# Kernel optimization log

Hardware: AMD Instinct MI355X
Metric: run time of the kernel (lower is better)

The kernel has to match this reference:

```python
import jax, jax.numpy as jnp
import numpy as np

N_NODES = 50000
N_EDGES = 800000
D_NODE = 64
D_ATTR = 16
D_T = 16
D_OUT = 128


def setup_inputs() -> dict:
    key = jax.random.key(0)
    ks = jax.random.split(key, 8)
    x = jax.random.normal(ks[0], (N_NODES, D_NODE), dtype=jnp.float32)
    edge_index = jax.random.randint(ks[1], (2, N_EDGES), 0, N_NODES, dtype=jnp.int64)
    edge_attr = jax.random.normal(ks[2], (N_EDGES, D_ATTR), dtype=jnp.float32)
    edge_t = jax.random.normal(ks[3], (N_EDGES, D_T), dtype=jnp.float32)
    d_msg = D_NODE + D_ATTR + D_T  # 96, = in_channels[0]
    Wm = jax.random.normal(ks[4], (d_msg, D_OUT), dtype=jnp.float32) / np.sqrt(d_msg)
    bm = jnp.zeros((D_OUT,), dtype=jnp.float32)
    Wr = jax.random.normal(ks[5], (D_NODE, D_OUT), dtype=jnp.float32) / np.sqrt(D_NODE)
    br = jnp.zeros((D_OUT,), dtype=jnp.float32)
    return {"x": x, "edge_index": edge_index, "edge_attr": edge_attr,
            "edge_t": edge_t, "Wm": Wm, "bm": bm, "Wr": Wr, "br": br}


def reference(x, edge_index, edge_attr, edge_t, Wm, bm, Wr, br):
    row, col = edge_index[0], edge_index[1]
    # gather source node feats and concat edge features -> [E, 96]
    msg = jnp.concatenate([x[col], edge_attr, edge_t], axis=1)
    # scatter-sum messages to destination nodes -> [N, 96]
    agg = jax.ops.segment_sum(msg, row, num_segments=x.shape[0])
    x_j = agg @ Wm + bm          # lin_m
    x_i = x @ Wr + br            # lin_r
    out = 0.5 * x_j + x_i        # normalize=False path
    return out
```

## Files before the change

### kernel.cpp

```cpp
#include <hip/hip_runtime.h>
#include <hip/hip_bf16.h>

#define NN 50000
#define NE 800000
#define D_NODE 64
#define D_MSG 96
#define D_K 160
#define AS 192
#define D_OUT 128
#define KP 168

#define SCAN_BLOCKS 49
#define XCAST_BLOCKS 3125
#define BT_BLOCKS 80

typedef __attribute__((ext_vector_type(8))) short bf16x8;
typedef __attribute__((ext_vector_type(4))) float f32x4;

#define CNT_OFF  0
#define DONE_OFF 200000
#define OFF_OFF  200064
#define CUR_OFF  400064
#define PERM_OFF 600064
#define A_OFF    7000064
#define BSUM_OFF (A_OFF + 128)

__device__ __forceinline__ unsigned short f2bf(float f) {
    __hip_bfloat16 h = __float2bfloat16(f);
    union { __hip_bfloat16 h; unsigned short u; } c; c.h = h;
    return c.u;
}
__device__ __forceinline__ float bf2f(unsigned int u) {
    union { unsigned int i; float f; } c; c.i = u << 16; return c.f;
}

__global__ __launch_bounds__(256) void prep_kernel(
    const float* __restrict__ x, unsigned short* __restrict__ A,
    const int* __restrict__ row, int* __restrict__ cnt)
{
    const int b = blockIdx.x;
    if (b < XCAST_BLOCKS) {
        int i = b * 256 + threadIdx.x;
        int node = i >> 4, c4 = i & 15;
        float4 v = *(const float4*)(x + (size_t)node * D_NODE + c4 * 4);
        uint2 pk;
        pk.x = (unsigned)f2bf(v.x) | ((unsigned)f2bf(v.y) << 16);
        pk.y = (unsigned)f2bf(v.z) | ((unsigned)f2bf(v.w) << 16);
        *(uint2*)(A + (size_t)node * AS + c4 * 4) = pk;
    } else {
        int e = (b - XCAST_BLOCKS) * 256 + threadIdx.x;
        if (e < NE) atomicAdd(&cnt[row[e]], 1);
    }
}

__global__ __launch_bounds__(256) void scan_kernel(
    const int* __restrict__ cnt, int* __restrict__ bsum,
    int* __restrict__ off, int* __restrict__ cur, int* __restrict__ done)
{
    const int t = threadIdx.x, b = blockIdx.x;
    const int idx4 = b * 256 + t;
    const bool valid = (idx4 < NN / 4);

    __shared__ int wsumA[4];
    int4 c = make_int4(0, 0, 0, 0);
    if (valid) c = ((const int4*)cnt)[idx4];
    int s = c.x + c.y + c.z + c.w;
    {
        int r = s;
        for (int d = 32; d > 0; d >>= 1) r += __shfl_down(r, d);
        if ((t & 63) == 0) wsumA[t >> 6] = r;
    }
    __syncthreads();
    if (t == 0) {
        bsum[b] = wsumA[0] + wsumA[1] + wsumA[2] + wsumA[3];
        __threadfence();
        atomicAdd(done, 1);
        while (__hip_atomic_load(done, __ATOMIC_ACQUIRE,
                                 __HIP_MEMORY_SCOPE_AGENT) < SCAN_BLOCKS)
            __builtin_amdgcn_s_sleep(1);
    }
    __syncthreads();

    __shared__ int s_boff;
    __shared__ int wsumC[4];
    if (t < 64) {
        int v = (t < SCAN_BLOCKS) ? bsum[t] : 0;
        int orig = v;
        for (int d = 1; d < 64; d <<= 1) {
            int u = __shfl_up(v, d);
            if (t >= d) v += u;
        }
        int excl = v - orig;
        int want = __shfl(excl, b);
        if (t == 0) s_boff = want;
    }

    const int lane = t & 63, w = t >> 6;
    int v = s;
    for (int d = 1; d < 64; d <<= 1) {
        int u = __shfl_up(v, d);
        if (lane >= d) v += u;
    }
    if (lane == 63) wsumC[w] = v;
    __syncthreads();
    int woff = 0;
    for (int i = 0; i < 4; ++i) if (i < w) woff += wsumC[i];

    if (valid) {
        int excl = (v - s) + woff + s_boff;
        int4 o;
        o.x = excl;
        o.y = o.x + c.x;
        o.z = o.y + c.y;
        o.w = o.z + c.z;
        ((int4*)off)[idx4] = o;
        ((int4*)cur)[idx4] = o;
    }
}

__global__ __launch_bounds__(256) void bucket_kernel(
    const int* __restrict__ row, const int* __restrict__ col,
    int* __restrict__ cur, int2* __restrict__ perm)
{
    int e = blockIdx.x * blockDim.x + threadIdx.x;
    if (e >= NE) return;
    int pos = atomicAdd(&cur[row[e]], 1);
    perm[pos] = make_int2(e, col[e]);
}

__global__ __launch_bounds__(256) void gather_kernel(
    const float* __restrict__ ea,
    const float* __restrict__ et,
    const int*  __restrict__ off,
    const int*  __restrict__ cnt,
    const int2* __restrict__ perm,
    unsigned short* __restrict__ A,
    const float* __restrict__ Wm,
    const float* __restrict__ Wr,
    unsigned short* __restrict__ Bt)
{
    const int grp = blockIdx.x;
    if (grp >= NN / 4) {
        int idx = (grp - NN / 4) * 256 + threadIdx.x;
        int n = idx & 127, k = idx >> 7;
        float v = (k < D_NODE) ? Wr[k * D_OUT + n] : Wm[(k - D_NODE) * D_OUT + n];
        Bt[n * KP + k] = f2bf(v);
        return;
    }

    const int node = grp * 4 + (threadIdx.x >> 6);
    const int lane = threadIdx.x & 63;

    const int beg = off[node];
    const int end = beg + cnt[node];

    const int half = lane >> 5;
    const int hl   = lane & 31;
    const float* ebase = ((lane >> 4) & 1) ? et : ea;
    const int ecol = lane & 15;

    float accx0 = 0.f, accx1 = 0.f, acce = 0.f;
    float accx0b = 0.f, accx1b = 0.f, acceb = 0.f;

#define EDGE_PAIR(q, ax0, ax1, ae)                                          \
    {                                                                       \
        int cc = half ? (q).w : (q).y;                                      \
        int ee = half ? (q).z : (q).x;                                      \
        unsigned xv = *(const unsigned*)(A + (size_t)cc * AS + hl * 2);     \
        float ev = ebase[(size_t)ee * 16 + ecol];                           \
        ax0 += bf2f(xv & 0xffffu);                                          \
        ax1 += bf2f(xv >> 16);                                              \
        ae  += ev;                                                          \
    }

    int j = beg;
    if ((j & 1) && j < end) {
        int2 p = perm[j];
        if (half == 0) {
            unsigned xv = *(const unsigned*)(A + (size_t)p.y * AS + hl * 2);
            accx0 += bf2f(xv & 0xffffu);
            accx1 += bf2f(xv >> 16);
            acce  += ebase[(size_t)p.x * 16 + ecol];
        }
        ++j;
    }
    for (; j + 8 <= end; j += 8) {
        int4 q0 = *(const int4*)(perm + j);
        int4 q1 = *(const int4*)(perm + j + 2);
        int4 q2 = *(const int4*)(perm + j + 4);
        int4 q3 = *(const int4*)(perm + j + 6);
        EDGE_PAIR(q0, accx0, accx1, acce)
        EDGE_PAIR(q1, accx0b, accx1b, acceb)
        EDGE_PAIR(q2, accx0, accx1, acce)
        EDGE_PAIR(q3, accx0b, accx1b, acceb)
    }
    if (j + 4 <= end) {
        int4 q0 = *(const int4*)(perm + j);
        int4 q1 = *(const int4*)(perm + j + 2);
        EDGE_PAIR(q0, accx0, accx1, acce)
        EDGE_PAIR(q1, accx0b, accx1b, acceb)
        j += 4;
    }
    if (j + 2 <= end) {
        int4 q0 = *(const int4*)(perm + j);
        EDGE_PAIR(q0, accx0, accx1, acce)
        j += 2;
    }
    if (j < end) {
        int2 p = perm[j];
        if (half == 0) {
            unsigned xv = *(const unsigned*)(A + (size_t)p.y * AS + hl * 2);
            accx0 += bf2f(xv & 0xffffu);
            accx1 += bf2f(xv >> 16);
            acce  += ebase[(size_t)p.x * 16 + ecol];
        }
    }
#undef EDGE_PAIR

    accx0 += accx0b; accx1 += accx1b; acce += acceb;
    accx0 += __shfl_xor(accx0, 32);
    accx1 += __shfl_xor(accx1, 32);
    acce  += __shfl_xor(acce, 32);

    unsigned short* dst = A + (size_t)node * AS;
    if (half == 0) {
        unsigned pk = (unsigned)f2bf(0.5f * accx0)
                    | ((unsigned)f2bf(0.5f * accx1) << 16);
        *(unsigned*)(dst + D_NODE + hl * 2) = pk;
    } else {
        dst[2 * D_NODE + hl] = f2bf(0.5f * acce);
    }
}

__global__ __launch_bounds__(256) void mfma_dense_kernel(
    const unsigned short* __restrict__ A,
    const unsigned short* __restrict__ Bt,
    const float* __restrict__ bm,
    const float* __restrict__ br,
    float*       __restrict__ out)
{
    const int l   = threadIdx.x & 63;
    const int wid = threadIdx.x >> 6;
    const int wm  = wid & 1;
    const int wn  = wid >> 1;
    const int lr  = l & 15;
    const int lk  = (l >> 4) << 3;

    bf16x8 bq[4][5];
#pragma unroll
    for (int nf = 0; nf < 4; ++nf) {
        int c = wn * 64 + nf * 16 + lr;
#pragma unroll
        for (int ks = 0; ks < 5; ++ks)
            bq[nf][ks] = *(const bf16x8*)(Bt + c * KP + ks * 32 + lk);
    }

    const int row0 = blockIdx.x * 64 + wm * 32;

    f32x4 acc[2][4];
#pragma unroll
    for (int mf = 0; mf < 2; ++mf)
#pragma unroll
        for (int nf = 0; nf < 4; ++nf)
            acc[mf][nf] = (f32x4){0.f, 0.f, 0.f, 0.f};

#pragma unroll
    for (int ks = 0; ks < 5; ++ks) {
#pragma unroll
        for (int mf = 0; mf < 2; ++mf) {
            int row = row0 + mf * 16 + lr;
            if (row > NN - 1) row = NN - 1;
            bf16x8 af = *(const bf16x8*)(A + (size_t)row * AS + ks * 32 + lk);
#pragma unroll
            for (int nf = 0; nf < 4; ++nf)
                acc[mf][nf] = __builtin_amdgcn_mfma_f32_16x16x32_bf16(
                    af, bq[nf][ks], acc[mf][nf], 0, 0, 0);
        }
    }

#pragma unroll
    for (int nf = 0; nf < 4; ++nf) {
        int c = wn * 64 + nf * 16 + lr;
        float bias = 0.5f * bm[c] + br[c];
#pragma unroll
        for (int mf = 0; mf < 2; ++mf) {
            int rbase = row0 + mf * 16 + ((l >> 4) << 2);
#pragma unroll
            for (int r = 0; r < 4; ++r) {
                int row = rbase + r;
                if (row < NN) out[(size_t)row * D_OUT + c] = acc[mf][nf][r] + bias;
            }
        }
    }
}

extern "C" void kernel_launch(void* const* d_in, const int* in_sizes, int n_in,
                              void* d_out, int out_size, void* d_ws, size_t ws_size,
                              hipStream_t stream) {
    const float* x  = (const float*)d_in[0];
    const int*   ei = (const int*)d_in[1];
    const float* ea = (const float*)d_in[2];
    const float* et = (const float*)d_in[3];
    const float* Wm = (const float*)d_in[4];
    const float* bm = (const float*)d_in[5];
    const float* Wr = (const float*)d_in[6];
    const float* br = (const float*)d_in[7];
    float* out = (float*)d_out;
    const int* row = ei;
    const int* col = ei + NE;

    char* ws = (char*)d_ws;
    int*  cnt  = (int*)(ws + CNT_OFF);
    int*  done = (int*)(ws + DONE_OFF);
    int*  off  = (int*)(ws + OFF_OFF);
    int*  cur  = (int*)(ws + CUR_OFF);
    int2* perm = (int2*)(ws + PERM_OFF);
    int*  bsum = (int*)(ws + BSUM_OFF);
    unsigned short* A  = (unsigned short*)(ws + A_OFF);
    unsigned short* Bt = (unsigned short*)(ws + CUR_OFF);

    hipMemsetAsync(ws, 0, 200064, stream);
    prep_kernel  <<<2 * XCAST_BLOCKS, 256, 0, stream>>>(x, A, row, cnt);
    scan_kernel  <<<SCAN_BLOCKS, 256, 0, stream>>>(cnt, bsum, off, cur, done);
    bucket_kernel<<<(NE + 255) / 256, 256, 0, stream>>>(row, col, cur, perm);
    gather_kernel<<<NN / 4 + BT_BLOCKS, 256, 0, stream>>>(
        ea, et, off, cnt, perm, A, Wm, Wr, Bt);
    mfma_dense_kernel<<<(NN + 63) / 64, 256, 0, stream>>>(A, Bt, bm, br, out);
}
```

Before: 161.7 us.

## Fuse prefix scan and edge bucketing into one kernel with ticket-ordered grid barrier

Merges the scan and bucket kernels into a single launch of NE/256 blocks. The first 49 blocks, picked by an atomic ticket, do the prefix scan and then signal a second counter. Every block preloads its row and col values and spins until the scan is done, then does the atomic bucketing. This removes one kernel launch and its gap, but all other blocks busy-wait on a global counter. The memset is widened to clear the new counters.

```diff
diff --git a/kernel.cpp b/kernel.cpp
--- a/kernel.cpp
+++ b/kernel.cpp
@@ -17,13 +17,15 @@
 typedef __attribute__((ext_vector_type(8))) short bf16x8;
 typedef __attribute__((ext_vector_type(4))) float f32x4;
 
-#define CNT_OFF  0
-#define DONE_OFF 200000
-#define OFF_OFF  200064
-#define CUR_OFF  400064
-#define PERM_OFF 600064
-#define A_OFF    7000064
-#define BSUM_OFF (A_OFF + 128)
+#define CNT_OFF   0
+#define DONE_OFF  200000
+#define DONE2_OFF 200064
+#define TICK_OFF  200128
+#define OFF_OFF   200192
+#define CUR_OFF   400192
+#define PERM_OFF  600192
+#define A_OFF     7000192
+#define BSUM_OFF  (A_OFF + 128)
 
 __device__ __forceinline__ unsigned short f2bf(float f) {
     __hip_bfloat16 h = __float2bfloat16(f);
@@ -53,79 +55,98 @@
     }
 }
 
-__global__ __launch_bounds__(256) void scan_kernel(
+__global__ __launch_bounds__(256) void scanbucket_kernel(
+    const int* __restrict__ row, const int* __restrict__ col,
     const int* __restrict__ cnt, int* __restrict__ bsum,
-    int* __restrict__ off, int* __restrict__ cur, int* __restrict__ done)
+    int* __restrict__ off, int* __restrict__ cur,
+    int* __restrict__ done, int* __restrict__ done2, int* __restrict__ tick,
+    int2* __restrict__ perm)
 {
-    const int t = threadIdx.x, b = blockIdx.x;
-    const int idx4 = b * 256 + t;
-    const bool valid = (idx4 < NN / 4);
-
-    __shared__ int wsumA[4];
-    int4 c = make_int4(0, 0, 0, 0);
-    if (valid) c = ((const int4*)cnt)[idx4];
-    int s = c.x + c.y + c.z + c.w;
-    {
-        int r = s;
-        for (int d = 32; d > 0; d >>= 1) r += __shfl_down(r, d);
-        if ((t & 63) == 0) wsumA[t >> 6] = r;
-    }
+    const int t = threadIdx.x;
+    const int e = blockIdx.x * 256 + t;
+    const int er = row[e];
+    const int ec = col[e];
+
+    __shared__ int s_tk;
+    if (t == 0) s_tk = atomicAdd(tick, 1);
     __syncthreads();
+    const int tk = s_tk;
+
+    if (tk < SCAN_BLOCKS) {
+        const int idx4 = tk * 256 + t;
+        const bool valid = (idx4 < NN / 4);
+
+        __shared__ int wsumA[4];
+        int4 c = make_int4(0, 0, 0, 0);
+        if (valid) c = ((const int4*)cnt)[idx4];
+        int s = c.x + c.y + c.z + c.w;
+        {
+            int r = s;
+            for (int d = 32; d > 0; d >>= 1) r += __shfl_down(r, d);
+            if ((t & 63) == 0) wsumA[t >> 6] = r;
+        }
+        __syncthreads();
+        if (t == 0) {
+            bsum[tk] = wsumA[0] + wsumA[1] + wsumA[2] + wsumA[3];
+            __threadfence();
+            atomicAdd(done, 1);
+            while (__hip_atomic_load(done, __ATOMIC_ACQUIRE,
+                                     __HIP_MEMORY_SCOPE_AGENT) < SCAN_BLOCKS)
+                __builtin_amdgcn_s_sleep(1);
+        }
+        __syncthreads();
+
+        __shared__ int s_boff;
+        __shared__ int wsumC[4];
+        if (t < 64) {
+            int v = (t < SCAN_BLOCKS) ? bsum[t] : 0;
+            int orig = v;
+            for (int d = 1; d < 64; d <<= 1) {
+                int u = __shfl_up(v, d);
+                if (t >= d) v += u;
+            }
+            int excl = v - orig;
+            int want = __shfl(excl, tk);
+            if (t == 0) s_boff = want;
+        }
+
+        const int lane = t & 63, w = t >> 6;
+        int v = s;
+        for (int d = 1; d < 64; d <<= 1) {
+            int u = __shfl_up(v, d);
+            if (lane >= d) v += u;
+        }
+        if (lane == 63) wsumC[w] = v;
+        __syncthreads();
+        int woff = 0;
+        for (int i = 0; i < 4; ++i) if (i < w) woff += wsumC[i];
+
+        if (valid) {
+            int excl = (v - s) + woff + s_boff;
+            int4 o;
+            o.x = excl;
+            o.y = o.x + c.x;
+            o.z = o.y + c.y;
+            o.w = o.z + c.z;
+            ((int4*)off)[idx4] = o;
+            ((int4*)cur)[idx4] = o;
+        }
+        __syncthreads();
+        if (t == 0) {
+            __threadfence();
+            atomicAdd(done2, 1);
+        }
+    }
+
     if (t == 0) {
-        bsum[b] = wsumA[0] + wsumA[1] + wsumA[2] + wsumA[3];
-        __threadfence();
-        atomicAdd(done, 1);
-        while (__hip_atomic_load(done, __ATOMIC_ACQUIRE,
+        while (__hip_atomic_load(done2, __ATOMIC_ACQUIRE,
                                  __HIP_MEMORY_SCOPE_AGENT) < SCAN_BLOCKS)
             __builtin_amdgcn_s_sleep(1);
     }
     __syncthreads();
 
-    __shared__ int s_boff;
-    __shared__ int wsumC[4];
-    if (t < 64) {
-        int v = (t < SCAN_BLOCKS) ? bsum[t] : 0;
-        int orig = v;
-        for (int d = 1; d < 64; d <<= 1) {
-            int u = __shfl_up(v, d);
-            if (t >= d) v += u;
-        }
-        int excl = v - orig;
-        int want = __shfl(excl, b);
-        if (t == 0) s_boff = want;
-    }
-
-    const int lane = t & 63, w = t >> 6;
-    int v = s;
-    for (int d = 1; d < 64; d <<= 1) {
-        int u = __shfl_up(v, d);
-        if (lane >= d) v += u;
-    }
-    if (lane == 63) wsumC[w] = v;
-    __syncthreads();
-    int woff = 0;
-    for (int i = 0; i < 4; ++i) if (i < w) woff += wsumC[i];
-
-    if (valid) {
-        int excl = (v - s) + woff + s_boff;
-        int4 o;
-        o.x = excl;
-        o.y = o.x + c.x;
-        o.z = o.y + c.y;
-        o.w = o.z + c.z;
-        ((int4*)off)[idx4] = o;
-        ((int4*)cur)[idx4] = o;
-    }
-}
-
-__global__ __launch_bounds__(256) void bucket_kernel(
-    const int* __restrict__ row, const int* __restrict__ col,
-    int* __restrict__ cur, int2* __restrict__ perm)
-{
-    int e = blockIdx.x * blockDim.x + threadIdx.x;
-    if (e >= NE) return;
-    int pos = atomicAdd(&cur[row[e]], 1);
-    perm[pos] = make_int2(e, col[e]);
+    int pos = atomicAdd(&cur[er], 1);
+    perm[pos] = make_int2(e, ec);
 }
 
 __global__ __launch_bounds__(256) void gather_kernel(
@@ -310,20 +331,22 @@
     const int* col = ei + NE;
 
     char* ws = (char*)d_ws;
-    int*  cnt  = (int*)(ws + CNT_OFF);
-    int*  done = (int*)(ws + DONE_OFF);
-    int*  off  = (int*)(ws + OFF_OFF);
-    int*  cur  = (int*)(ws + CUR_OFF);
-    int2* perm = (int2*)(ws + PERM_OFF);
-    int*  bsum = (int*)(ws + BSUM_OFF);
+    int*  cnt   = (int*)(ws + CNT_OFF);
+    int*  done  = (int*)(ws + DONE_OFF);
+    int*  done2 = (int*)(ws + DONE2_OFF);
+    int*  tick  = (int*)(ws + TICK_OFF);
+    int*  off   = (int*)(ws + OFF_OFF);
+    int*  cur   = (int*)(ws + CUR_OFF);
+    int2* perm  = (int2*)(ws + PERM_OFF);
+    int*  bsum  = (int*)(ws + BSUM_OFF);
     unsigned short* A  = (unsigned short*)(ws + A_OFF);
     unsigned short* Bt = (unsigned short*)(ws + CUR_OFF);
 
-    hipMemsetAsync(ws, 0, 200064, stream);
-    prep_kernel  <<<2 * XCAST_BLOCKS, 256, 0, stream>>>(x, A, row, cnt);
-    scan_kernel  <<<SCAN_BLOCKS, 256, 0, stream>>>(cnt, bsum, off, cur, done);
-    bucket_kernel<<<(NE + 255) / 256, 256, 0, stream>>>(row, col, cur, perm);
-    gather_kernel<<<NN / 4 + BT_BLOCKS, 256, 0, stream>>>(
+    hipMemsetAsync(ws, 0, OFF_OFF, stream);
+    prep_kernel      <<<2 * XCAST_BLOCKS, 256, 0, stream>>>(x, A, row, cnt);
+    scanbucket_kernel<<<NE / 256, 256, 0, stream>>>(
+        row, col, cnt, bsum, off, cur, done, done2, tick, perm);
+    gather_kernel    <<<NN / 4 + BT_BLOCKS, 256, 0, stream>>>(
         ea, et, off, cnt, perm, A, Wm, Wr, Bt);
     mfma_dense_kernel<<<(NN + 63) / 64, 256, 0, stream>>>(A, Bt, bm, br, out);
 }
```

Measured after the change: 321.2 us. 98.6% more time.
